# Performance work log

Hardware: AMD Instinct MI355X
Metric: run time of the kernel (lower is better)

Reference implementation:

```python
import jax, jax.numpy as jnp
import numpy as np

CONF_THRES = 0.25
IOU_THRES = 0.45
MAX_DET = 300      # max detections returned (padded/masked to static shape)
K = 8192           # top-K score candidates entering NMS (static bound)
N_ANCHORS = 102000 # YOLOv5 @ 1280px
NC = 80            # COCO classes


def setup_inputs() -> dict:
    key = jax.random.key(0)
    # [B=1, N, 4 (xywh) + 1 (obj) + 80 (cls)] raw head predictions in [0,1)
    preds = jax.random.uniform(key, (1, N_ANCHORS, 4 + 1 + NC), dtype=jnp.float32)
    return {"preds": preds}


def _xywh2yxyx(b):
    # (xc, yc, w, h) -> (y1, x1, y2, x2), matching pt_xywh2yxyx_yolo
    x, y, w, h = b[..., 0], b[..., 1], b[..., 2], b[..., 3]
    return jnp.stack([y - h * 0.5, x - w * 0.5, y + h * 0.5, x + w * 0.5], axis=-1)


def _iou_matrix(boxes):
    # boxes: [K, 4] in yxyx; returns pairwise IoU [K, K]
    area = (boxes[:, 2] - boxes[:, 0]) * (boxes[:, 3] - boxes[:, 1])
    ty = jnp.maximum(boxes[:, None, 0], boxes[None, :, 0])
    tx = jnp.maximum(boxes[:, None, 1], boxes[None, :, 1])
    by = jnp.minimum(boxes[:, None, 2], boxes[None, :, 2])
    bx = jnp.minimum(boxes[:, None, 3], boxes[None, :, 3])
    inter = jnp.clip(by - ty, 0.0) * jnp.clip(bx - tx, 0.0)
    union = area[:, None] + area[None, :] - inter
    return inter / (union + 1e-9)


def _yolo_nms(preds):
    p = preds[0]                       # [N, 85] (loop returns on first image)
    obj = p[:, 4]                      # objectness
    cand = obj > CONF_THRES            # confidence filter
    cls_scores = p[:, 5:] * obj[:, None]
    scores = jnp.max(cls_scores, axis=1)
    classes = jnp.argmax(cls_scores, axis=1).astype(jnp.float32)
    scores = jnp.where(cand, scores, 0.0)  # mask instead of dynamic filter
    boxes = _xywh2yxyx(p[:, :4])       # [N, 4] yxyx

    # top-K candidates by score (static replacement for boolean filtering)
    top_scores, idx = jax.lax.top_k(scores, K)
    top_boxes = boxes[idx]
    top_classes = classes[idx]
    valid = top_scores > 0.0

    iou = _iou_matrix(top_boxes)       # [K, K], 256 MB fp32

    # greedy NMS: boxes already sorted by descending score
    ar = jnp.arange(K)

    def body(i, suppressed):
        keep_i = jnp.logical_and(jnp.logical_not(suppressed[i]), valid[i])
        return suppressed | (keep_i & (iou[i] > IOU_THRES) & (ar > i))

    suppressed = jax.lax.fori_loop(0, K, body, jnp.zeros((K,), jnp.bool_))
    keep = valid & jnp.logical_not(suppressed)

    # gather top MAX_DET kept detections (sorted), zero-pad the rest
    keep_scores = jnp.where(keep, top_scores, -1.0)
    _, sel = jax.lax.top_k(keep_scores, MAX_DET)
    mask = keep[sel]
    out_boxes = jnp.where(mask[:, None], top_boxes[sel], 0.0)[None]    # [1, MAX_DET, 4]
    out_classes = jnp.where(mask, top_classes[sel], 0.0)[None]         # [1, MAX_DET]
    out_scores = jnp.where(mask, top_scores[sel], 0.0)[None]           # [1, MAX_DET]
    return out_boxes, out_classes, out_scores


def reference(preds):
    return _yolo_nms(preds)
```

## Files before the change

### kernel.cpp

```cpp
#include <hip/hip_runtime.h>
#include <cstdint>

#define CONF_THRES 0.25f
#define IOU_THRES  0.45f
#define MAX_DET    300
#define K_TOP      8192
#define NA         102000
#define NCLS       80
#define ROWLEN     85
#define CAP        32640
#define NPLANE     32
#define NBINS      16384
#define WIN        512
#define NWIN       (K_TOP / WIN)
#define SSTR       9

typedef unsigned long long u64;
typedef unsigned int u32;

__global__ __launch_bounds__(256) void zero_kernel(uint4* __restrict__ a,
        uint4* __restrict__ r, uint4* __restrict__ b) {
    int i = blockIdx.x * 256 + threadIdx.x;
    uint4 z = make_uint4(0u, 0u, 0u, 0u);
    if (i < 4164) a[i] = z;
    if (i < 8160) r[i] = z;
    b[i] = z;
    b[i + 65536] = z;
}

__global__ __launch_bounds__(256) void score_key_kernel(const float* __restrict__ preds,
        u64* __restrict__ keys, u32* __restrict__ histP) {
#pragma clang fp contract(off)
    int lane = threadIdx.x & 63;
    int i = blockIdx.x * 4 + (threadIdx.x >> 6);
    if (i >= NA) return;
    const float* p = preds + (size_t)i * ROWLEN;
    float v0 = p[lane];
    float v1 = (lane < ROWLEN - 64) ? p[64 + lane] : 0.0f;
    float obj = __shfl(v0, 4);
    float m = (lane >= 5) ? v0 : 0.0f;
    m = fmaxf(m, (lane < 21) ? v1 : 0.0f);
    for (int off = 32; off; off >>= 1) m = fmaxf(m, __shfl_xor(m, off));
    if (lane == 0) {
        float score = (obj > CONF_THRES) ? m * obj : 0.0f;
        u32 sb = __float_as_uint(score);
        keys[i] = ((u64)sb << 32) | (u32)(~(u32)i);
        if (sb != 0u)
            atomicAdd(&histP[((u32)blockIdx.x & (NPLANE - 1u)) * NBINS + (sb >> 16)], 1u);
    }
}

__global__ __launch_bounds__(256) void reduce_hist_kernel(const u32* __restrict__ histP,
        u32* __restrict__ sumhist) {
    int bin = blockIdx.x * 256 + threadIdx.x;
    u32 s = 0;
#pragma unroll
    for (int r = 0; r < NPLANE; ++r) s += histP[r * NBINS + bin];
    sumhist[bin] = s;
}

__global__ __launch_bounds__(1024) void cutoff_kernel(const u32* __restrict__ hist,
        u32* __restrict__ meta) {
    __shared__ u32 suf[1024];
    __shared__ int cbs;
    __shared__ u32 above_s;
    int t = threadIdx.x;
    u32 s = 0;
    const u32* hb = hist + t * 16;
    for (int b = 0; b < 16; ++b) s += hb[b];
    suf[t] = s;
    if (t == 0) { cbs = -1; above_s = 0; }
    __syncthreads();
    for (int off = 1; off < 1024; off <<= 1) {
        u32 add = (t + off < 1024) ? suf[t + off] : 0u;
        __syncthreads();
        suf[t] += add;
        __syncthreads();
    }
    u32 st = suf[t];
    u32 stn = (t < 1023) ? suf[t + 1] : 0u;
    if (st >= (u32)K_TOP && stn < (u32)K_TOP) {
        cbs = t;
        above_s = stn;
    }
    __syncthreads();
    int cb = cbs;
    if (t < 64) {
        u32 thresh = 0;
        if (cb >= 0) {
            u32 above = above_s;
            u32 v = (t < 16) ? hist[cb * 16 + t] : 0u;
            for (int off = 1; off < 64; off <<= 1) {
                u32 o = __shfl_down(v, off);
                if (t + off < 64) v += o;
            }
            u64 bal = __ballot(v + above >= (u32)K_TOP);
            int bstar = 63 - __builtin_clzll((unsigned long long)bal);
            thresh = ((u32)(cb * 16 + bstar)) << 16;
        }
        if (t == 0) meta[1] = thresh;
    }
}

__global__ __launch_bounds__(256) void compact_kernel(const u64* __restrict__ keys,
        u32* __restrict__ meta, u64* __restrict__ comp) {
    __shared__ u32 woff[4];
    __shared__ u32 bbase;
    int i = blockIdx.x * 256 + threadIdx.x;
    int wid = threadIdx.x >> 6, lane = threadIdx.x & 63;
    u64 key = (i < NA) ? keys[i] : 0ull;
    u32 sb = (u32)(key >> 32);
    u32 th = meta[1];
    bool take = (i < NA) && (sb != 0u) && (sb >= th);
    u64 bal = __ballot(take);
    if (lane == 0) woff[wid] = (u32)__popcll(bal);
    __syncthreads();
    if (threadIdx.x == 0) {
        u32 t0 = woff[0], t1 = woff[1], t2 = woff[2], t3 = woff[3];
        bbase = atomicAdd(&meta[0], t0 + t1 + t2 + t3);
        woff[0] = 0; woff[1] = t0; woff[2] = t0 + t1; woff[3] = t0 + t1 + t2;
    }
    __syncthreads();
    if (take) {
        u32 pos = bbase + woff[wid] + (u32)__popcll(bal & ((1ull << lane) - 1ull));
        if (pos < CAP) comp[pos] = key;
    }
}

__global__ __launch_bounds__(256) void rank_partial_kernel(const u64* __restrict__ comp,
        const u32* __restrict__ meta, u32* __restrict__ rankArr) {
    __shared__ u64 tile[1024];
    u32 cnt = meta[0];
    int n = (int)(cnt < (u32)CAP ? cnt : (u32)CAP);
    int i0 = blockIdx.x * 256;
    int j0 = blockIdx.y * 1024;
    if (i0 >= n || j0 >= n) return;
    int lim = n - j0; if (lim > 1024) lim = 1024;
    for (int k = threadIdx.x; k < 1024; k += 256)
        tile[k] = (k < lim) ? comp[j0 + k] : 0ull;
    __syncthreads();
    int i = i0 + threadIdx.x;
    if (i < n) {
        u64 key = comp[i];
        u32 r = 0;
#pragma unroll 8
        for (int j = 0; j < 1024; ++j) r += (tile[j] > key) ? 1u : 0u;
        atomicAdd(&rankArr[i], r);
    }
}

__global__ __launch_bounds__(256) void scatter_kernel(const u64* __restrict__ comp,
        const u32* __restrict__ meta, const u32* __restrict__ rankArr,
        u64* __restrict__ sorted) {
    u32 cnt = meta[0];
    int n = (int)(cnt < (u32)CAP ? cnt : (u32)CAP);
    int i = blockIdx.x * 256 + threadIdx.x;
    if (i < n) {
        u32 r = rankArr[i];
        if (r < (u32)K_TOP) sorted[r] = comp[i];
    }
}

__global__ __launch_bounds__(256) void gather_kernel(const u64* __restrict__ sorted,
        const float* __restrict__ preds, float* __restrict__ boxes,
        float* __restrict__ scores, float* __restrict__ classes,
        float* __restrict__ areas) {
#pragma clang fp contract(off)
    int lane = threadIdx.x & 63;
    int i = blockIdx.x * 4 + (threadIdx.x >> 6);
    u64 key = sorted[i];
    u32 sb = (u32)(key >> 32);
    float score = __uint_as_float(sb);
    if (score > 0.0f) {
        u32 idx = ~(u32)(key & 0xffffffffull);
        const float* p = preds + (size_t)idx * ROWLEN;
        float v0 = p[lane];
        float v1 = (lane < ROWLEN - 64) ? p[64 + lane] : 0.0f;
        float obj = __shfl(v0, 4);
        u64 kb = 0;
        if (lane >= 5) {
            float q = v0 * obj;
            kb = ((u64)__float_as_uint(q) << 8) | (u32)(255 - (lane - 5));
        }
        if (lane < 21) {
            float q = v1 * obj;
            u64 kb2 = ((u64)__float_as_uint(q) << 8) | (u32)(255 - (59 + lane));
            if (kb2 > kb) kb = kb2;
        }
        for (int off = 32; off; off >>= 1) {
            u64 o = __shfl_xor(kb, off);
            if (o > kb) kb = o;
        }
        u32 cls = 255u - (u32)(kb & 0xffull);
        float x = __shfl(v0, 0), y = __shfl(v0, 1);
        float w = __shfl(v0, 2), h = __shfl(v0, 3);
        if (lane == 0) {
            float ymin = y - h * 0.5f, xmin = x - w * 0.5f;
            float ymax = y + h * 0.5f, xmax = x + w * 0.5f;
            boxes[i * 4 + 0] = ymin;
            boxes[i * 4 + 1] = xmin;
            boxes[i * 4 + 2] = ymax;
            boxes[i * 4 + 3] = xmax;
            scores[i] = score;
            classes[i] = (float)cls;
            areas[i] = (ymax - ymin) * (xmax - xmin);
        }
    } else if (lane == 0) {
        boxes[i * 4 + 0] = 0.0f; boxes[i * 4 + 1] = 0.0f;
        boxes[i * 4 + 2] = 0.0f; boxes[i * 4 + 3] = 0.0f;
        scores[i] = 0.0f;
        classes[i] = 0.0f;
        areas[i] = 0.0f;
    }
}

__global__ __launch_bounds__(256) void mask_kernel(const float* __restrict__ boxes,
        const float* __restrict__ areas, u64* __restrict__ mask) {
#pragma clang fp contract(off)
    int cx = blockIdx.x;
    int ry = blockIdx.y;
    if (cx < (ry >> 2)) return;
    __shared__ u64 st[64 * 5];
    int wv = threadIdx.x >> 6, lane = threadIdx.x & 63;
    int jw = cx * 4 + wv;
    int j  = jw * 64 + lane;
    int r0 = ry * 64;
    int jb = jw * 64;
    float4 bj = ((const float4*)boxes)[j];
    float aj = areas[j];
    float4 bi = ((const float4*)boxes)[r0 + lane];
    float ai = areas[r0 + lane];
    u64 myword = 0;
#pragma unroll
    for (int rr = 0; rr < 64; ++rr) {
        float sx = __int_as_float(__builtin_amdgcn_readlane(__float_as_int(bi.x), rr));
        float sy = __int_as_float(__builtin_amdgcn_readlane(__float_as_int(bi.y), rr));
        float sz = __int_as_float(__builtin_amdgcn_readlane(__float_as_int(bi.z), rr));
        float sw = __int_as_float(__builtin_amdgcn_readlane(__float_as_int(bi.w), rr));
        float sa = __int_as_float(__builtin_amdgcn_readlane(__float_as_int(ai), rr));
        float ty = fmaxf(sx, bj.x);
        float tx = fmaxf(sy, bj.y);
        float by = fminf(sz, bj.z);
        float bx = fminf(sw, bj.w);
        float inter = fmaxf(by - ty, 0.0f) * fmaxf(bx - tx, 0.0f);
        float uni = (sa + aj) - inter;
        float iou = inter / (uni + 1e-9f);
        u64 bal = __ballot(iou > IOU_THRES);
        int d = (r0 + rr) - jb;
        u64 vm = (d < 0) ? ~0ull : ((d >= 63) ? 0ull : (~0ull << (d + 1)));
        bal &= vm;
        if (lane == rr) myword = bal;
    }
    st[lane * 5 + wv] = myword;
    __syncthreads();
    int t = threadIdx.x;
    mask[(size_t)(r0 + (t >> 2)) * 128 + cx * 4 + (t & 3)] = st[(t >> 2) * 5 + (t & 3)];
}

__global__ __launch_bounds__(256) void valid_kernel(const float* __restrict__ scores,
        u64* __restrict__ remw) {
    int w = blockIdx.x * 4 + (threadIdx.x >> 6);
    int lane = threadIdx.x & 63;
    u64 b = __ballot(scores[w * 64 + lane] > 0.0f);
    if (lane == 0) remw[w] = b;
}

__device__ __forceinline__ u64 rfl64(u64 v) {
    u32 lo = (u32)__builtin_amdgcn_readfirstlane((int)(u32)v);
    u32 hi = (u32)__builtin_amdgcn_readfirstlane((int)(u32)(v >> 32));
    return ((u64)hi << 32) | lo;
}

__device__ __forceinline__ u64 bcast64(u64 v, int srclane) {
    u32 lo = (u32)__builtin_amdgcn_readlane((int)(u32)v, srclane);
    u32 hi = (u32)__builtin_amdgcn_readlane((int)(u32)(v >> 32), srclane);
    return ((u64)hi << 32) | lo;
}

__device__ __forceinline__ u64 shfl_xor64(u64 v, int m) {
    u32 lo = __shfl_xor((u32)v, m, 64);
    u32 hi = __shfl_xor((u32)(v >> 32), m, 64);
    return ((u64)hi << 32) | lo;
}

__global__ __launch_bounds__(64) void nms_scan_kernel(const u64* __restrict__ mask,
        const u64* __restrict__ remw, const float* __restrict__ boxes,
        const float* __restrict__ scores, const float* __restrict__ classes,
        float* __restrict__ out) {
    __shared__ u64 sub[WIN * SSTR];
    __shared__ u32 ki[MAX_DET + 8];
    int lane = threadIdx.x;
    int n = 0;
    for (int win = 0; win < NWIN && n < MAX_DET; ++win) {
        int rbase = win * WIN;
        __syncthreads();
#pragma unroll 8
        for (int it = 0; it < 32; ++it) {
            int idx = it * 64 + lane;
            int r = idx >> 2, j = (idx & 3) * 2;
            uint4 v = *(const uint4*)&mask[(size_t)(rbase + r) * 128 + win * 8 + j];
            sub[r * SSTR + j]     = ((u64)v.y << 32) | v.x;
            sub[r * SSTR + j + 1] = ((u64)v.w << 32) | v.z;
        }
        u64 acc[8] = {0, 0, 0, 0, 0, 0, 0, 0};
        for (int m = lane; m < n; m += 64) {
            int k = (int)ki[m];
            const u64* rp = &mask[(size_t)k * 128 + win * 8];
#pragma unroll
            for (int j = 0; j < 8; ++j) acc[j] |= rp[j];
        }
#pragma unroll
        for (int j = 0; j < 8; ++j)
            for (int off = 32; off; off >>= 1) acc[j] |= shfl_xor64(acc[j], off);
        __syncthreads();
        u64 diag[8];
#pragma unroll
        for (int sw = 0; sw < 8; ++sw) diag[sw] = sub[(sw * 64 + lane) * SSTR + sw];
        int n0 = n;
        u64 keptW[8] = {0, 0, 0, 0, 0, 0, 0, 0};
#pragma unroll
        for (int sw = 0; sw < 8; ++sw) {
            if (n < MAX_DET) {
                u64 acc2 = 0;
#pragma unroll
                for (int wp = 0; wp < 8; ++wp) {
                    if (wp < sw) {
                        if ((keptW[wp] >> lane) & 1ull)
                            acc2 |= sub[(wp * 64 + lane) * SSTR + sw];
                    }
                }
                for (int off = 32; off; off >>= 1) acc2 |= shfl_xor64(acc2, off);
                u64 cur = rfl64(remw[win * 8 + sw]) & ~rfl64(acc[sw]) & ~rfl64(acc2);
                u64 kw = 0;
                while (cur != 0ull && n < MAX_DET) {
                    int b = __ffsll((unsigned long long)cur) - 1;
                    u64 slice = bcast64(diag[sw], b);
                    kw |= (1ull << b);
                    cur &= ~(slice | (1ull << b));
                    ++n;
                }
                keptW[sw] = kw;
            }
        }
        int base = n0;
#pragma unroll
        for (int sw = 0; sw < 8; ++sw) {
            u64 kw = keptW[sw];
            if ((kw >> lane) & 1ull) {
                int rr = (int)__popcll(kw & ((1ull << lane) - 1ull));
                ki[base + rr] = (u32)(rbase + sw * 64 + lane);
            }
            base += (int)__popcll(kw);
        }
        __syncthreads();
    }
    __syncthreads();
    for (int m = lane; m < MAX_DET; m += 64) {
        float4 b = make_float4(0.0f, 0.0f, 0.0f, 0.0f);
        float c = 0.0f, s = 0.0f;
        if (m < n) {
            int k = (int)ki[m];
            b = ((const float4*)boxes)[k];
            c = classes[k];
            s = scores[k];
        }
        ((float4*)out)[m] = b;
        out[1200 + m] = c;
        out[1500 + m] = s;
    }
}

extern "C" void kernel_launch(void* const* d_in, const int* in_sizes, int n_in,
                              void* d_out, int out_size, void* d_ws, size_t ws_size,
                              hipStream_t stream) {
    const float* preds = (const float*)d_in[0];
    char* ws = (char*)d_ws;

    u32*   sumhist = (u32*)(ws + 0);
    u32*   rankArr = (u32*)(ws + 65536);
    u32*   meta    = (u32*)(ws + 262144);
    u64*   remw    = (u64*)(ws + 262208);
    u64*   sorted  = (u64*)(ws + 263232);
    u64*   keys    = (u64*)(ws + 328768);
    u64*   comp    = (u64*)(ws + 1144768);
    float* careas  = (float*)(ws + 1144768);
    float* tboxes  = (float*)(ws + 1405888);
    float* tscores = (float*)(ws + 1536960);
    float* tclass  = (float*)(ws + 1569728);
    u64*   mask    = (u64*)(ws + 1602496);
    u32*   histP   = (u32*)(ws + 1602496);
    float* out     = (float*)d_out;

    zero_kernel<<<256, 256, 0, stream>>>((uint4*)(ws + 262144), (uint4*)rankArr,
            (uint4*)histP);
    score_key_kernel<<<(NA + 3) / 4, 256, 0, stream>>>(preds, keys, histP);
    reduce_hist_kernel<<<64, 256, 0, stream>>>(histP, sumhist);
    cutoff_kernel<<<1, 1024, 0, stream>>>(sumhist, meta);
    compact_kernel<<<(NA + 255) / 256, 256, 0, stream>>>(keys, meta, comp);
    rank_partial_kernel<<<dim3((CAP + 255) / 256, (CAP + 1023) / 1024), 256, 0, stream>>>(
            comp, meta, rankArr);
    scatter_kernel<<<(CAP + 255) / 256, 256, 0, stream>>>(comp, meta, rankArr, sorted);
    gather_kernel<<<K_TOP / 4, 256, 0, stream>>>(sorted, preds, tboxes, tscores,
            tclass, careas);
    mask_kernel<<<dim3(32, 128), 256, 0, stream>>>(tboxes, careas, mask);
    valid_kernel<<<32, 256, 0, stream>>>(tscores, remw);
    nms_scan_kernel<<<1, 64, 0, stream>>>(mask, remw, tboxes, tscores, tclass, out);
}
```

Before: 230.5 us.

## Restructure IoU mask kernel with LDS column tiles, division-free compare, fused validity

Each block now stages its 256 column boxes in shared memory. Every lane builds its own 64-bit suppression word by looping over columns, replacing the per-row readlane broadcasts and ballots. The IoU division becomes a double-precision multiply-compare against a slightly padded threshold, and wavefronts that lie entirely below the diagonal skip their computation. The separate validity-ballot kernel is folded into the diagonal blocks, which saves one launch. The double-precision comparison costs throughput and may differ from the float division right at the threshold boundary.

```diff
diff --git a/kernel.cpp b/kernel.cpp
--- a/kernel.cpp
+++ b/kernel.cpp
@@ -215,54 +215,53 @@
 }
 
 __global__ __launch_bounds__(256) void mask_kernel(const float* __restrict__ boxes,
-        const float* __restrict__ areas, u64* __restrict__ mask) {
+        const float* __restrict__ areas, const float* __restrict__ scores,
+        u64* __restrict__ mask, u64* __restrict__ remw) {
 #pragma clang fp contract(off)
     int cx = blockIdx.x;
     int ry = blockIdx.y;
     if (cx < (ry >> 2)) return;
+    __shared__ float4 cb[256];
+    __shared__ float  ca[256];
     __shared__ u64 st[64 * 5];
-    int wv = threadIdx.x >> 6, lane = threadIdx.x & 63;
+    int tid = threadIdx.x;
+    int wv = tid >> 6, lane = tid & 63;
+    int r0 = ry * 64;
     int jw = cx * 4 + wv;
-    int j  = jw * 64 + lane;
-    int r0 = ry * 64;
-    int jb = jw * 64;
-    float4 bj = ((const float4*)boxes)[j];
-    float aj = areas[j];
-    float4 bi = ((const float4*)boxes)[r0 + lane];
-    float ai = areas[r0 + lane];
+    cb[tid] = ((const float4*)boxes)[cx * 256 + tid];
+    ca[tid] = areas[cx * 256 + tid];
+    if (cx == (ry >> 2) && wv == 0) {
+        u64 b = __ballot(scores[r0 + lane] > 0.0f);
+        if (lane == 0) remw[ry] = b;
+    }
+    __syncthreads();
     u64 myword = 0;
-#pragma unroll
-    for (int rr = 0; rr < 64; ++rr) {
-        float sx = __int_as_float(__builtin_amdgcn_readlane(__float_as_int(bi.x), rr));
-        float sy = __int_as_float(__builtin_amdgcn_readlane(__float_as_int(bi.y), rr));
-        float sz = __int_as_float(__builtin_amdgcn_readlane(__float_as_int(bi.z), rr));
-        float sw = __int_as_float(__builtin_amdgcn_readlane(__float_as_int(bi.w), rr));
-        float sa = __int_as_float(__builtin_amdgcn_readlane(__float_as_int(ai), rr));
-        float ty = fmaxf(sx, bj.x);
-        float tx = fmaxf(sy, bj.y);
-        float by = fminf(sz, bj.z);
-        float bx = fminf(sw, bj.w);
-        float inter = fmaxf(by - ty, 0.0f) * fmaxf(bx - tx, 0.0f);
-        float uni = (sa + aj) - inter;
-        float iou = inter / (uni + 1e-9f);
-        u64 bal = __ballot(iou > IOU_THRES);
-        int d = (r0 + rr) - jb;
-        u64 vm = (d < 0) ? ~0ull : ((d >= 63) ? 0ull : (~0ull << (d + 1)));
-        bal &= vm;
-        if (lane == rr) myword = bal;
+    if (jw >= ry) {
+        float4 bi = ((const float4*)boxes)[r0 + lane];
+        float ai = areas[r0 + lane];
+        const double Bd = (double)IOU_THRES + 0x1p-26;
+        int kb = wv * 64;
+#pragma unroll
+        for (int k = 0; k < 64; ++k) {
+            float4 bj = cb[kb + k];
+            float aj = ca[kb + k];
+            float ty = fmaxf(bi.x, bj.x);
+            float tx = fmaxf(bi.y, bj.y);
+            float by = fminf(bi.z, bj.z);
+            float bx = fminf(bi.w, bj.w);
+            float inter = fmaxf(by - ty, 0.0f) * fmaxf(bx - tx, 0.0f);
+            float uni = (ai + aj) - inter;
+            float u = uni + 1e-9f;
+            bool sup = ((double)inter > Bd * (double)u);
+            myword |= sup ? (1ull << k) : 0ull;
+        }
+        if (jw == ry)
+            myword &= (lane < 63) ? (~0ull << (lane + 1)) : 0ull;
     }
     st[lane * 5 + wv] = myword;
     __syncthreads();
-    int t = threadIdx.x;
-    mask[(size_t)(r0 + (t >> 2)) * 128 + cx * 4 + (t & 3)] = st[(t >> 2) * 5 + (t & 3)];
-}
-
-__global__ __launch_bounds__(256) void valid_kernel(const float* __restrict__ scores,
-        u64* __restrict__ remw) {
-    int w = blockIdx.x * 4 + (threadIdx.x >> 6);
-    int lane = threadIdx.x & 63;
-    u64 b = __ballot(scores[w * 64 + lane] > 0.0f);
-    if (lane == 0) remw[w] = b;
+    mask[(size_t)(r0 + (tid >> 2)) * 128 + cx * 4 + (tid & 3)] =
+            st[(tid >> 2) * 5 + (tid & 3)];
 }
 
 __device__ __forceinline__ u64 rfl64(u64 v) {
@@ -402,7 +401,6 @@
     scatter_kernel<<<(CAP + 255) / 256, 256, 0, stream>>>(comp, meta, rankArr, sorted);
     gather_kernel<<<K_TOP / 4, 256, 0, stream>>>(sorted, preds, tboxes, tscores,
             tclass, careas);
-    mask_kernel<<<dim3(32, 128), 256, 0, stream>>>(tboxes, careas, mask);
-    valid_kernel<<<32, 256, 0, stream>>>(tscores, remw);
+    mask_kernel<<<dim3(32, 128), 256, 0, stream>>>(tboxes, careas, tscores, mask, remw);
     nms_scan_kernel<<<1, 64, 0, stream>>>(mask, remw, tboxes, tscores, tclass, out);
 }
```

Result: faster. 196.4 us (-14.8%).
